# Kernel tuning notes

Measured on AMD Instinct MI355X. Metric: run time of the kernel, lower is better.

Reference implementation:

```python
import jax, jax.numpy as jnp
import numpy as np

EPS = 1e-5  # torch BatchNorm1d default eps

def lrelu(v):
    # LeakyReLU(0.2)
    return jnp.where(v >= 0, v, 0.2 * v)

def setup_inputs() -> dict:
    key = jax.random.key(0)
    ks = jax.random.split(key, 5)
    B, C, N = 32, 64, 1024  # batch, in_features(=out_features), num_nodes
    def w(k, shape, scale):
        return (jax.random.normal(k, shape) * scale).astype(jnp.float32)
    return {
        "x": jax.random.normal(ks[0], (B, C, N), jnp.float32),
        # static_adj: Conv1d(N, N, 1, bias=False) -> weight [N, N]
        "W_sa": w(ks[1], (N, N), 0.02),
        # static_weight: Conv1d(C, C, 1) -> weight [C, C], bias [C]
        "W_sw": w(ks[2], (C, C), 0.1),
        "b_sw": jnp.zeros((C,), jnp.float32),
        # bn: BatchNorm1d(64) affine params (training-mode batch stats used)
        "bn_gamma": jnp.ones((C,), jnp.float32),
        "bn_beta": jnp.zeros((C,), jnp.float32),
        # gamma parameter (init 0 in torch; set 0.5 so the attention path is live)
        "gamma": jnp.full((1,), 0.5, jnp.float32),
        # conv_create_co_mat: Conv1d(C, N, 1) -> weight [N, C], bias [N]
        "W_cm": w(ks[3], (N, C), 0.1),
        "b_cm": jnp.zeros((N,), jnp.float32),
        # dynamic_weight: Conv1d(C, C, 1) -> weight [C, C], bias [C]
        "W_dw": w(ks[4], (C, C), 0.1),
        "b_dw": jnp.zeros((C,), jnp.float32),
    }

def reference(x, W_sa, W_sw, b_sw, bn_gamma, bn_beta, gamma, W_cm, b_cm, W_dw, b_dw):
    # x: [B, C, N]
    # ---- static GCN: adj mix over nodes, then 1x1 conv over channels ----
    t = lrelu(jnp.einsum('mn,bcn->bcm', W_sa, x))                     # [B, C, N]
    out_static = lrelu(jnp.einsum('oc,bcn->bon', W_sw, t) + b_sw[None, :, None])
    x1 = x + out_static                                               # [B, C, N]
    # ---- construct dynamic graph ----
    energy = jnp.einsum('bcn,bdn->bcd', x, x)                         # [B, C, C]
    energy_new = jnp.max(energy, axis=-1, keepdims=True) - energy     # [B, C, C]
    # BatchNorm1d(64) in training mode: batch stats over (B, last) per channel
    mu = jnp.mean(energy_new, axis=(0, 2), keepdims=True)
    var = jnp.var(energy_new, axis=(0, 2), keepdims=True)
    attention = bn_gamma[None, :, None] * (energy_new - mu) * jax.lax.rsqrt(var + EPS) + bn_beta[None, :, None]
    out = jnp.einsum('bcd,bdn->bcn', attention, x)                    # [B, C, N]
    x_glb = gamma * out + x
    dyn_adj = jax.nn.sigmoid(jnp.einsum('mc,bcn->bmn', W_cm, x_glb) + b_cm[None, :, None])  # [B, N, N]
    # ---- dynamic GCN ----
    y = lrelu(jnp.einsum('bcn,bnm->bcm', x1, dyn_adj))                # [B, C, N]
    y = lrelu(jnp.einsum('oc,bcn->bon', W_dw, y) + b_dw[None, :, None])
    return y
```

## Files before the change

### kernel.cpp

```cpp
#include <hip/hip_runtime.h>
#include <hip/hip_bf16.h>

#define Bv 32
#define Cv 64
#define Nv 1024

typedef __attribute__((ext_vector_type(8))) short bf16x8;
typedef __attribute__((ext_vector_type(4))) float f32x4;
typedef __attribute__((ext_vector_type(8))) unsigned short us8;
typedef __attribute__((ext_vector_type(4))) unsigned short us4;

__device__ __forceinline__ float lrelu(float v) { return v >= 0.f ? v : 0.2f * v; }
__device__ __forceinline__ float sigmoidf_(float z) {
  return __builtin_amdgcn_rcpf(1.f + __expf(-z));
}
__device__ __forceinline__ unsigned short f2bh(float f) {
  __hip_bfloat16 h = __float2bfloat16(f);
  return reinterpret_cast<unsigned short&>(h);
}
__device__ __forceinline__ void gload16(const void* g, void* l) {
  __builtin_amdgcn_global_load_lds((const __attribute__((address_space(1))) void*)g,
                                   (__attribute__((address_space(3))) void*)l, 16, 0, 0);
}
__device__ __forceinline__ void stage_tile(const unsigned short* src, size_t stride,
                                           unsigned short* dst, int wave, int lane) {
#pragma unroll
  for (int p = 0; p < 2; ++p) {
    int q = wave * 2 + p;
    int rr = q * 8 + (lane >> 3);
    int gS = ((lane & 7) ^ (rr & 7)) << 3;
    gload16(&src[(size_t)rr * stride + gS], &dst[q * 512]);
  }
}
__device__ __forceinline__ bf16x8 fragr(const unsigned short* buf, int row, int ks, int lane) {
  return *reinterpret_cast<const bf16x8*>(
      &buf[row * 64 + (((ks * 4 + (lane >> 4)) ^ (row & 7)) << 3)]);
}

__device__ __forceinline__ void cvt8(const float* in, unsigned short* out, int i) {
  const f32x4* p = reinterpret_cast<const f32x4*>(in + (size_t)i * 8);
  f32x4 a = p[0], b = p[1];
  us8 o;
  o[0] = f2bh(a[0]); o[1] = f2bh(a[1]); o[2] = f2bh(a[2]); o[3] = f2bh(a[3]);
  o[4] = f2bh(b[0]); o[5] = f2bh(b[1]); o[6] = f2bh(b[2]); o[7] = f2bh(b[3]);
  *reinterpret_cast<us8*>(out + (size_t)i * 8) = o;
}

__global__ __launch_bounds__(256)
void prep_kernel(const float* __restrict__ x, const float* __restrict__ Wsa,
                 const float* __restrict__ Wcm, const float* __restrict__ Wsw,
                 const float* __restrict__ Wdw, unsigned short* __restrict__ xb,
                 unsigned short* __restrict__ xbT, unsigned short* __restrict__ WsaB,
                 unsigned short* __restrict__ WcmB, unsigned short* __restrict__ WswB,
                 unsigned short* __restrict__ WdwB) {
  __shared__ unsigned short L[64 * 72];
  const int blk = blockIdx.x, tid = threadIdx.x;
  if (blk < 512) {
    int b = blk >> 4, n0 = (blk & 15) * 64;
    int c = tid >> 2, nseg = (tid & 3) * 16;
    const float* src = &x[((size_t)(b * 64 + c) << 10) + n0 + nseg];
    unsigned short v16[16];
#pragma unroll
    for (int q = 0; q < 4; ++q) {
      f32x4 v = *reinterpret_cast<const f32x4*>(src + q * 4);
#pragma unroll
      for (int e = 0; e < 4; ++e) {
        unsigned short bf = f2bh(v[e]);
        v16[q * 4 + e] = bf;
        L[(nseg + q * 4 + e) * 72 + c] = bf;
      }
    }
    unsigned short* sd = &xb[((size_t)(b * 64 + c) << 10) + n0 + nseg];
    *reinterpret_cast<us8*>(sd) = *reinterpret_cast<const us8*>(&v16[0]);
    *reinterpret_cast<us8*>(sd + 8) = *reinterpret_cast<const us8*>(&v16[8]);
    __syncthreads();
    int n = tid >> 2, cs = (tid & 3) * 16;
    us8 a = *reinterpret_cast<const us8*>(&L[n * 72 + cs]);
    us8 bq = *reinterpret_cast<const us8*>(&L[n * 72 + cs + 8]);
    unsigned short* dst = &xbT[(((size_t)b << 10) + n0 + n) * 64 + cs];
    *reinterpret_cast<us8*>(dst) = a;
    *reinterpret_cast<us8*>(dst + 8) = bq;
  } else if (blk < 1024) {
    cvt8(Wsa, WsaB, (blk - 512) * 256 + tid);
  } else if (blk < 1056) {
    cvt8(Wcm, WcmB, (blk - 1024) * 256 + tid);
  } else if (blk < 1058) {
    cvt8(Wsw, WswB, (blk - 1056) * 256 + tid);
  } else {
    cvt8(Wdw, WdwB, (blk - 1058) * 256 + tid);
  }
}

__global__ __launch_bounds__(256)
void k1x1_kernel(const unsigned short* __restrict__ xb,
                 const unsigned short* __restrict__ WsaB,
                 const unsigned short* __restrict__ WswB,
                 const float* __restrict__ x, const float* __restrict__ bsw,
                 unsigned short* __restrict__ x1b, float* __restrict__ en) {
  __shared__ __align__(16) unsigned short As[2][4096];
  __shared__ __align__(16) unsigned short Bs[2][4096];
  __shared__ __align__(16) unsigned short TT[64 * 72];
  __shared__ __align__(16) float Xres[64 * 68];
  const int tid = threadIdx.x, wave = tid >> 6, lane = tid & 63;
  const int b = blockIdx.y, col0 = blockIdx.x * 64, row0 = b * 64;
  const int wr = wave >> 1, wc = wave & 1;
  const bool doEn = (blockIdx.x == 0);
  f32x4 acc[2][2], accE[4];
#pragma unroll
  for (int i = 0; i < 2; ++i)
#pragma unroll
    for (int j = 0; j < 2; ++j) acc[i][j] = (f32x4){0.f, 0.f, 0.f, 0.f};
#pragma unroll
  for (int j = 0; j < 4; ++j) accE[j] = (f32x4){0.f, 0.f, 0.f, 0.f};

  stage_tile(&xb[(size_t)row0 * Nv], Nv, As[0], wave, lane);
  stage_tile(&WsaB[(size_t)col0 * Nv], Nv, Bs[0], wave, lane);
  __syncthreads();
  for (int t = 0; t < 16; ++t) {
    const int cur = t & 1;
    if (t < 15) {
      stage_tile(&xb[(size_t)row0 * Nv + (t + 1) * 64], Nv, As[cur ^ 1], wave, lane);
      stage_tile(&WsaB[(size_t)col0 * Nv + (t + 1) * 64], Nv, Bs[cur ^ 1], wave, lane);
    }
#pragma unroll
    for (int ks = 0; ks < 2; ++ks) {
      bf16x8 af[2], bfg[2];
#pragma unroll
      for (int i = 0; i < 2; ++i) af[i] = fragr(As[cur], wr * 32 + i * 16 + (lane & 15), ks, lane);
#pragma unroll
      for (int j = 0; j < 2; ++j) bfg[j] = fragr(Bs[cur], wc * 32 + j * 16 + (lane & 15), ks, lane);
#pragma unroll
      for (int i = 0; i < 2; ++i)
#pragma unroll
        for (int j = 0; j < 2; ++j)
          acc[i][j] = __builtin_amdgcn_mfma_f32_16x16x32_bf16(af[i], bfg[j], acc[i][j], 0, 0, 0);
      if (doEn) {
        bf16x8 aE = fragr(As[cur], wave * 16 + (lane & 15), ks, lane);
#pragma unroll
        for (int j = 0; j < 4; ++j) {
          bf16x8 bE = fragr(As[cur], j * 16 + (lane & 15), ks, lane);
          accE[j] = __builtin_amdgcn_mfma_f32_16x16x32_bf16(aE, bE, accE[j], 0, 0, 0);
        }
      }
    }
    __syncthreads();
  }
#pragma unroll
  for (int i = 0; i < 2; ++i)
#pragma unroll
    for (int j = 0; j < 2; ++j) {
      us4 tv;
#pragma unroll
      for (int r = 0; r < 4; ++r) tv[r] = f2bh(lrelu(acc[i][j][r]));
      *reinterpret_cast<us4*>(
          &TT[(wc * 32 + j * 16 + (lane & 15)) * 72 + wr * 32 + i * 16 + (lane >> 4) * 4]) = tv;
    }
  {
    int o = tid >> 2, ms = (tid & 3) * 16;
    const float* xs = &x[((size_t)(row0 + o) << 10) + col0 + ms];
#pragma unroll
    for (int q = 0; q < 4; ++q)
      *reinterpret_cast<f32x4*>(&Xres[o * 68 + ms + q * 4]) =
          *reinterpret_cast<const f32x4*>(xs + q * 4);
  }
  if (doEn) {
#pragma unroll
    for (int j = 0; j < 4; ++j)
#pragma unroll
      for (int r = 0; r < 4; ++r)
        en[(size_t)b * 4096 + (wave * 16 + (lane >> 4) * 4 + r) * 64 + j * 16 + (lane & 15)] =
            accE[j][r];
  }
  __syncthreads();
  bf16x8 afw[2];
#pragma unroll
  for (int ks = 0; ks < 2; ++ks)
    afw[ks] = *reinterpret_cast<const bf16x8*>(
        &WswB[(wave * 16 + (lane & 15)) * 64 + ks * 32 + (lane >> 4) * 8]);
  f32x4 acc2[4];
#pragma unroll
  for (int j = 0; j < 4; ++j) acc2[j] = (f32x4){0.f, 0.f, 0.f, 0.f};
#pragma unroll
  for (int ks = 0; ks < 2; ++ks)
#pragma unroll
    for (int j = 0; j < 4; ++j) {
      bf16x8 bfr = *reinterpret_cast<const bf16x8*>(
          &TT[(j * 16 + (lane & 15)) * 72 + ks * 32 + (lane >> 4) * 8]);
      acc2[j] = __builtin_amdgcn_mfma_f32_16x16x32_bf16(afw[ks], bfr, acc2[j], 0, 0, 0);
    }
  f32x4 bs4 = *reinterpret_cast<const f32x4*>(&bsw[wave * 16 + (lane >> 4) * 4]);
#pragma unroll
  for (int j = 0; j < 4; ++j)
#pragma unroll
    for (int r = 0; r < 4; ++r) {
      int o = wave * 16 + (lane >> 4) * 4 + r;
      int nl = j * 16 + (lane & 15);
      x1b[((size_t)(row0 + o) << 10) + col0 + nl] =
          f2bh(Xres[o * 68 + nl] + lrelu(acc2[j][r] + bs4[r]));
    }
}

__global__ __launch_bounds__(64)
void bn_att_kernel(const float* __restrict__ en, const float* __restrict__ bng,
                   const float* __restrict__ bnb, unsigned short* __restrict__ att) {
  const int c = blockIdx.x, d = threadIdx.x;
  float v[Bv];
  float sum = 0.f, sumsq = 0.f;
#pragma unroll
  for (int b = 0; b < Bv; ++b) {
    float e = en[(size_t)b * 4096 + c * 64 + d];
    float m = e;
#pragma unroll
    for (int o = 32; o > 0; o >>= 1) m = fmaxf(m, __shfl_xor(m, o));
    v[b] = m - e;
    sum += v[b]; sumsq += v[b] * v[b];
  }
#pragma unroll
  for (int o = 32; o > 0; o >>= 1) { sum += __shfl_xor(sum, o); sumsq += __shfl_xor(sumsq, o); }
  const float inv = 1.f / (float)(Bv * Cv);
  float mu = sum * inv;
  float var = sumsq * inv - mu * mu;
  float rs = rsqrtf(var + 1e-5f);
  float g = bng[c], be = bnb[c];
#pragma unroll
  for (int b = 0; b < Bv; ++b)
    att[(size_t)b * 4096 + c * 64 + d] = f2bh(g * (v[b] - mu) * rs + be);
}

__global__ __launch_bounds__(256)
void dynmega_kernel(const unsigned short* __restrict__ xbT,
                    const unsigned short* __restrict__ x1b,
                    const unsigned short* __restrict__ attB,
                    const unsigned short* __restrict__ WcmB,
                    const unsigned short* __restrict__ WdwB,
                    const float* __restrict__ x, const float* __restrict__ bcm,
                    const float* __restrict__ bdw, const float* __restrict__ gamma_p,
                    float* __restrict__ dout) {
  __shared__ __align__(16) unsigned short XG[64 * 72];
  __shared__ __align__(16) char buf[32768];
  __shared__ __align__(16) unsigned short SBt[4 * 16 * 72];
  const int tid = threadIdx.x, wave = tid >> 6, lane = tid & 63;
  const int m0 = blockIdx.x * 64, b = blockIdx.y;
  {
    unsigned short* XB = (unsigned short*)buf;
    float* Xr = (float*)(buf + 8192);
    stage_tile(&xbT[((size_t)b * 1024 + m0) * 64], 64, XB, wave, lane);
    {
      int o = tid >> 2, ms = (tid & 3) * 16;
      const float* xs = &x[((size_t)(b * 64 + o) << 10) + m0 + ms];
#pragma unroll
      for (int q = 0; q < 4; ++q)
        *reinterpret_cast<f32x4*>(&Xr[o * 68 + ms + q * 4]) =
            *reinterpret_cast<const f32x4*>(xs + q * 4);
    }
    __syncthreads();
    bf16x8 afA[2];
#pragma unroll
    for (int ks = 0; ks < 2; ++ks)
      afA[ks] = *reinterpret_cast<const bf16x8*>(
          &attB[(size_t)b * 4096 + (wave * 16 + (lane & 15)) * 64 + ks * 32 + (lane >> 4) * 8]);
    const float g0 = gamma_p[0];
#pragma unroll
    for (int j = 0; j < 4; ++j) {
      f32x4 ah = (f32x4){0.f, 0.f, 0.f, 0.f};
#pragma unroll
      for (int ks = 0; ks < 2; ++ks) {
        bf16x8 bfh = fragr(XB, j * 16 + (lane & 15), ks, lane);
        ah = __builtin_amdgcn_mfma_f32_16x16x32_bf16(afA[ks], bfh, ah, 0, 0, 0);
      }
      us4 gv;
#pragma unroll
      for (int r = 0; r < 4; ++r)
        gv[r] =
            f2bh(g0 * ah[r] + Xr[(wave * 16 + (lane >> 4) * 4 + r) * 68 + j * 16 + (lane & 15)]);
      *reinterpret_cast<us4*>(
          &XG[(j * 16 + (lane & 15)) * 72 + wave * 16 + (lane >> 4) * 4]) = gv;
    }
  }
  __syncthreads();
  bf16x8 xgf[2];
#pragma unroll
  for (int ks = 0; ks < 2; ++ks)
    xgf[ks] = *reinterpret_cast<const bf16x8*>(
        &XG[(wave * 16 + (lane & 15)) * 72 + ks * 32 + (lane >> 4) * 8]);
  stage_tile(&WcmB[0], 64, (unsigned short*)buf, wave, lane);
  stage_tile(&x1b[(size_t)b * 65536], 1024, (unsigned short*)(buf + 8192), wave, lane);
  __syncthreads();
  f32x4 accy[4];
#pragma unroll
  for (int j = 0; j < 4; ++j) accy[j] = (f32x4){0.f, 0.f, 0.f, 0.f};
  unsigned short* SB = &SBt[wave * 16 * 72];

  auto chunk_body = [&](const char* base, int ch) {
    const unsigned short* WTcur = (const unsigned short*)base;
    const unsigned short* X1cur = (const unsigned short*)(base + 8192);
#pragma unroll
    for (int i = 0; i < 4; ++i) {
      f32x4 s = (f32x4){0.f, 0.f, 0.f, 0.f};
#pragma unroll
      for (int ks = 0; ks < 2; ++ks) {
        bf16x8 af = fragr(WTcur, i * 16 + (lane & 15), ks, lane);
        s = __builtin_amdgcn_mfma_f32_16x16x32_bf16(af, xgf[ks], s, 0, 0, 0);
      }
      f32x4 bc4 = *reinterpret_cast<const f32x4*>(&bcm[ch * 64 + i * 16 + (lane >> 4) * 4]);
      us4 sv;
#pragma unroll
      for (int r = 0; r < 4; ++r) sv[r] = f2bh(sigmoidf_(s[r] + bc4[r]));
      *reinterpret_cast<us4*>(&SB[(lane & 15) * 72 + i * 16 + (lane >> 4) * 4]) = sv;
    }
#pragma unroll
    for (int ks = 0; ks < 2; ++ks) {
      bf16x8 b2 = *reinterpret_cast<const bf16x8*>(
          &SB[(lane & 15) * 72 + ks * 32 + (lane >> 4) * 8]);
#pragma unroll
      for (int jc = 0; jc < 4; ++jc) {
        bf16x8 a2 = fragr(X1cur, jc * 16 + (lane & 15), ks, lane);
        accy[jc] = __builtin_amdgcn_mfma_f32_16x16x32_bf16(a2, b2, accy[jc], 0, 0, 0);
      }
    }
  };

  for (int hp = 0; hp < 8; ++hp) {
    {
      const int ch = hp * 2;
      stage_tile(&WcmB[(size_t)(ch + 1) * 4096], 64, (unsigned short*)(buf + 16384), wave, lane);
      stage_tile(&x1b[(size_t)b * 65536 + (ch + 1) * 64], 1024,
                 (unsigned short*)(buf + 16384 + 8192), wave, lane);
      chunk_body(buf, ch);
      __syncthreads();
    }
    {
      const int ch = hp * 2 + 1;
      if (hp < 7) {
        stage_tile(&WcmB[(size_t)(ch + 1) * 4096], 64, (unsigned short*)buf, wave, lane);
        stage_tile(&x1b[(size_t)b * 65536 + (ch + 1) * 64], 1024,
                   (unsigned short*)(buf + 8192), wave, lane);
      }
      chunk_body(buf + 16384, ch);
      __syncthreads();
    }
  }
  unsigned short* YT = SB;
#pragma unroll
  for (int jc = 0; jc < 4; ++jc) {
    us4 yv;
#pragma unroll
    for (int r = 0; r < 4; ++r) yv[r] = f2bh(lrelu(accy[jc][r]));
    *reinterpret_cast<us4*>(&YT[(lane & 15) * 72 + jc * 16 + (lane >> 4) * 4]) = yv;
  }
  bf16x8 afW[4][2];
#pragma unroll
  for (int jo = 0; jo < 4; ++jo)
#pragma unroll
    for (int ks = 0; ks < 2; ++ks)
      afW[jo][ks] = *reinterpret_cast<const bf16x8*>(
          &WdwB[(jo * 16 + (lane & 15)) * 64 + ks * 32 + (lane >> 4) * 8]);
  f32x4 accf[4];
#pragma unroll
  for (int j = 0; j < 4; ++j) accf[j] = (f32x4){0.f, 0.f, 0.f, 0.f};
#pragma unroll
  for (int ks = 0; ks < 2; ++ks) {
    bf16x8 yf = *reinterpret_cast<const bf16x8*>(
        &YT[(lane & 15) * 72 + ks * 32 + (lane >> 4) * 8]);
#pragma unroll
    for (int jo = 0; jo < 4; ++jo)
      accf[jo] = __builtin_amdgcn_mfma_f32_16x16x32_bf16(afW[jo][ks], yf, accf[jo], 0, 0, 0);
  }
#pragma unroll
  for (int jo = 0; jo < 4; ++jo) {
    f32x4 bs4 = *reinterpret_cast<const f32x4*>(&bdw[jo * 16 + (lane >> 4) * 4]);
#pragma unroll
    for (int r = 0; r < 4; ++r) {
      int o = jo * 16 + (lane >> 4) * 4 + r;
      dout[((size_t)(b * 64 + o) << 10) + m0 + wave * 16 + (lane & 15)] =
          lrelu(accf[jo][r] + bs4[r]);
    }
  }
}

extern "C" void kernel_launch(void* const* d_in, const int* in_sizes, int n_in,
                              void* d_out, int out_size, void* d_ws, size_t ws_size,
                              hipStream_t stream) {
  const float* x     = (const float*)d_in[0];
  const float* W_sa  = (const float*)d_in[1];
  const float* W_sw  = (const float*)d_in[2];
  const float* b_sw  = (const float*)d_in[3];
  const float* bn_g  = (const float*)d_in[4];
  const float* bn_b  = (const float*)d_in[5];
  const float* gamma = (const float*)d_in[6];
  const float* W_cm  = (const float*)d_in[7];
  const float* b_cm  = (const float*)d_in[8];
  const float* W_dw  = (const float*)d_in[9];
  const float* b_dw  = (const float*)d_in[10];
  float* out = (float*)d_out;

  char* ws = (char*)d_ws;
  const size_t MB = 1024 * 1024;
  unsigned short* xb     = (unsigned short*)(ws + 0 * MB);
  unsigned short* xbT    = (unsigned short*)(ws + 4 * MB);
  unsigned short* WsaB   = (unsigned short*)(ws + 8 * MB);
  unsigned short* WcmB   = (unsigned short*)(ws + 10 * MB);
  unsigned short* WswB   = (unsigned short*)(ws + 10 * MB + 256 * 1024);
  unsigned short* WdwB   = (unsigned short*)(ws + 10 * MB + 288 * 1024);
  unsigned short* x1b    = (unsigned short*)(ws + 11 * MB);
  float*          en     = (float*)(ws + 15 * MB);
  unsigned short* attB   = (unsigned short*)(ws + 16 * MB);

  prep_kernel<<<1060, 256, 0, stream>>>(x, W_sa, W_cm, W_sw, W_dw, xb, xbT, WsaB, WcmB, WswB,
                                        WdwB);
  k1x1_kernel<<<dim3(16, Bv), 256, 0, stream>>>(xb, WsaB, WswB, x, b_sw, x1b, en);
  bn_att_kernel<<<Cv, 64, 0, stream>>>(en, bn_g, bn_b, attB);
  dynmega_kernel<<<dim3(16, Bv), 256, 0, stream>>>(xbT, x1b, attB, WcmB, WdwB, x, b_cm, b_dw,
                                                   gamma, out);
}
```

Baseline: 58.93 us.

## Widen dynamic GCN block to 128 nodes with 8 waves sharing staged tiles

The dynamic megakernel now runs 512 threads per block covering 128 output nodes instead of 64. The staged W_cm and x1 chunk tiles are shared by twice as many waves, which halves redundant global and LDS staging per output. LDS padding is replaced by XOR swizzle so the larger buffers fit, and the residual x is read directly from global memory instead of being staged in LDS. The grid halves to 256 blocks, which may lower occupancy across CUs, and the uncoalesced direct x loads could cost bandwidth.

```diff
diff --git a/kernel.cpp b/kernel.cpp
--- a/kernel.cpp
+++ b/kernel.cpp
@@ -32,9 +32,18 @@
     gload16(&src[(size_t)rr * stride + gS], &dst[q * 512]);
   }
 }
+__device__ __forceinline__ void stage_tile8(const unsigned short* src, size_t stride,
+                                            unsigned short* dst, int wave, int lane) {
+  int rr = wave * 8 + (lane >> 3);
+  int gS = ((lane & 7) ^ (rr & 7)) << 3;
+  gload16(&src[(size_t)rr * stride + gS], &dst[wave * 512]);
+}
 __device__ __forceinline__ bf16x8 fragr(const unsigned short* buf, int row, int ks, int lane) {
   return *reinterpret_cast<const bf16x8*>(
       &buf[row * 64 + (((ks * 4 + (lane >> 4)) ^ (row & 7)) << 3)]);
+}
+__device__ __forceinline__ void swz_store4(unsigned short* buf, int row, int col, us4 v) {
+  *reinterpret_cast<us4*>(&buf[row * 64 + (((col >> 3) ^ (row & 7)) << 3) + (col & 7)]) = v;
 }
 
 __device__ __forceinline__ void cvt8(const float* in, unsigned short* out, int i) {
@@ -227,7 +236,7 @@
     att[(size_t)b * 4096 + c * 64 + d] = f2bh(g * (v[b] - mu) * rs + be);
 }
 
-__global__ __launch_bounds__(256)
+__global__ __launch_bounds__(512)
 void dynmega_kernel(const unsigned short* __restrict__ xbT,
                     const unsigned short* __restrict__ x1b,
                     const unsigned short* __restrict__ attB,
@@ -236,60 +245,55 @@
                     const float* __restrict__ x, const float* __restrict__ bcm,
                     const float* __restrict__ bdw, const float* __restrict__ gamma_p,
                     float* __restrict__ dout) {
-  __shared__ __align__(16) unsigned short XG[64 * 72];
+  __shared__ __align__(16) unsigned short XG[128 * 64];
   __shared__ __align__(16) char buf[32768];
-  __shared__ __align__(16) unsigned short SBt[4 * 16 * 72];
+  __shared__ __align__(16) unsigned short SBt[8 * 16 * 64];
   const int tid = threadIdx.x, wave = tid >> 6, lane = tid & 63;
-  const int m0 = blockIdx.x * 64, b = blockIdx.y;
+  const int M0 = blockIdx.x * 128, b = blockIdx.y;
   {
     unsigned short* XB = (unsigned short*)buf;
-    float* Xr = (float*)(buf + 8192);
-    stage_tile(&xbT[((size_t)b * 1024 + m0) * 64], 64, XB, wave, lane);
-    {
-      int o = tid >> 2, ms = (tid & 3) * 16;
-      const float* xs = &x[((size_t)(b * 64 + o) << 10) + m0 + ms];
-#pragma unroll
-      for (int q = 0; q < 4; ++q)
-        *reinterpret_cast<f32x4*>(&Xr[o * 68 + ms + q * 4]) =
-            *reinterpret_cast<const f32x4*>(xs + q * 4);
-    }
+    stage_tile8(&xbT[((size_t)b * 1024 + M0) * 64], 64, XB, wave, lane);
+    stage_tile8(&xbT[((size_t)b * 1024 + M0 + 64) * 64], 64, XB + 4096, wave, lane);
     __syncthreads();
+    const int cs = (wave & 3) * 16, mt = wave >> 2;
+    const unsigned short* XBm = XB + mt * 4096;
     bf16x8 afA[2];
 #pragma unroll
     for (int ks = 0; ks < 2; ++ks)
       afA[ks] = *reinterpret_cast<const bf16x8*>(
-          &attB[(size_t)b * 4096 + (wave * 16 + (lane & 15)) * 64 + ks * 32 + (lane >> 4) * 8]);
+          &attB[(size_t)b * 4096 + (cs + (lane & 15)) * 64 + ks * 32 + (lane >> 4) * 8]);
     const float g0 = gamma_p[0];
 #pragma unroll
     for (int j = 0; j < 4; ++j) {
       f32x4 ah = (f32x4){0.f, 0.f, 0.f, 0.f};
 #pragma unroll
       for (int ks = 0; ks < 2; ++ks) {
-        bf16x8 bfh = fragr(XB, j * 16 + (lane & 15), ks, lane);
+        bf16x8 bfh = fragr(XBm, j * 16 + (lane & 15), ks, lane);
         ah = __builtin_amdgcn_mfma_f32_16x16x32_bf16(afA[ks], bfh, ah, 0, 0, 0);
       }
+      const int mrow = mt * 64 + j * 16 + (lane & 15);
       us4 gv;
 #pragma unroll
-      for (int r = 0; r < 4; ++r)
-        gv[r] =
-            f2bh(g0 * ah[r] + Xr[(wave * 16 + (lane >> 4) * 4 + r) * 68 + j * 16 + (lane & 15)]);
-      *reinterpret_cast<us4*>(
-          &XG[(j * 16 + (lane & 15)) * 72 + wave * 16 + (lane >> 4) * 4]) = gv;
+      for (int r = 0; r < 4; ++r) {
+        int c = cs + (lane >> 4) * 4 + r;
+        float xr = x[((size_t)(b * 64 + c) << 10) + M0 + mrow];
+        gv[r] = f2bh(g0 * ah[r] + xr);
+      }
+      swz_store4(XG, mrow, cs + (lane >> 4) * 4, gv);
     }
   }
   __syncthreads();
   bf16x8 xgf[2];
 #pragma unroll
   for (int ks = 0; ks < 2; ++ks)
-    xgf[ks] = *reinterpret_cast<const bf16x8*>(
-        &XG[(wave * 16 + (lane & 15)) * 72 + ks * 32 + (lane >> 4) * 8]);
-  stage_tile(&WcmB[0], 64, (unsigned short*)buf, wave, lane);
-  stage_tile(&x1b[(size_t)b * 65536], 1024, (unsigned short*)(buf + 8192), wave, lane);
+    xgf[ks] = fragr(XG, wave * 16 + (lane & 15), ks, lane);
+  stage_tile8(&WcmB[0], 64, (unsigned short*)buf, wave, lane);
+  stage_tile8(&x1b[(size_t)b * 65536], 1024, (unsigned short*)(buf + 8192), wave, lane);
   __syncthreads();
   f32x4 accy[4];
 #pragma unroll
   for (int j = 0; j < 4; ++j) accy[j] = (f32x4){0.f, 0.f, 0.f, 0.f};
-  unsigned short* SB = &SBt[wave * 16 * 72];
+  unsigned short* SB = &SBt[wave * 1024];
 
   auto chunk_body = [&](const char* base, int ch) {
     const unsigned short* WTcur = (const unsigned short*)base;
@@ -306,12 +310,11 @@
       us4 sv;
 #pragma unroll
       for (int r = 0; r < 4; ++r) sv[r] = f2bh(sigmoidf_(s[r] + bc4[r]));
-      *reinterpret_cast<us4*>(&SB[(lane & 15) * 72 + i * 16 + (lane >> 4) * 4]) = sv;
+      swz_store4(SB, lane & 15, i * 16 + (lane >> 4) * 4, sv);
     }
 #pragma unroll
     for (int ks = 0; ks < 2; ++ks) {
-      bf16x8 b2 = *reinterpret_cast<const bf16x8*>(
-          &SB[(lane & 15) * 72 + ks * 32 + (lane >> 4) * 8]);
+      bf16x8 b2 = fragr(SB, lane & 15, ks, lane);
 #pragma unroll
       for (int jc = 0; jc < 4; ++jc) {
         bf16x8 a2 = fragr(X1cur, jc * 16 + (lane & 15), ks, lane);
@@ -323,30 +326,29 @@
   for (int hp = 0; hp < 8; ++hp) {
     {
       const int ch = hp * 2;
-      stage_tile(&WcmB[(size_t)(ch + 1) * 4096], 64, (unsigned short*)(buf + 16384), wave, lane);
-      stage_tile(&x1b[(size_t)b * 65536 + (ch + 1) * 64], 1024,
-                 (unsigned short*)(buf + 16384 + 8192), wave, lane);
+      stage_tile8(&WcmB[(size_t)(ch + 1) * 4096], 64, (unsigned short*)(buf + 16384), wave, lane);
+      stage_tile8(&x1b[(size_t)b * 65536 + (ch + 1) * 64], 1024,
+                  (unsigned short*)(buf + 16384 + 8192), wave, lane);
       chunk_body(buf, ch);
       __syncthreads();
     }
     {
       const int ch = hp * 2 + 1;
       if (hp < 7) {
-        stage_tile(&WcmB[(size_t)(ch + 1) * 4096], 64, (unsigned short*)buf, wave, lane);
-        stage_tile(&x1b[(size_t)b * 65536 + (ch + 1) * 64], 1024,
-                   (unsigned short*)(buf + 8192), wave, lane);
+        stage_tile8(&WcmB[(size_t)(ch + 1) * 4096], 64, (unsigned short*)buf, wave, lane);
+        stage_tile8(&x1b[(size_t)b * 65536 + (ch + 1) * 64], 1024,
+                    (unsigned short*)(buf + 8192), wave, lane);
       }
       chunk_body(buf + 16384, ch);
       __syncthreads();
     }
   }
-  unsigned short* YT = SB;
 #pragma unroll
   for (int jc = 0; jc < 4; ++jc) {
     us4 yv;
 #pragma unroll
     for (int r = 0; r < 4; ++r) yv[r] = f2bh(lrelu(accy[jc][r]));
-    *reinterpret_cast<us4*>(&YT[(lane & 15) * 72 + jc * 16 + (lane >> 4) * 4]) = yv;
+    swz_store4(SB, lane & 15, jc * 16 + (lane >> 4) * 4, yv);
   }
   bf16x8 afW[4][2];
 #pragma unroll
@@ -360,8 +362,7 @@
   for (int j = 0; j < 4; ++j) accf[j] = (f32x4){0.f, 0.f, 0.f, 0.f};
 #pragma unroll
   for (int ks = 0; ks < 2; ++ks) {
-    bf16x8 yf = *reinterpret_cast<const bf16x8*>(
-        &YT[(lane & 15) * 72 + ks * 32 + (lane >> 4) * 8]);
+    bf16x8 yf = fragr(SB, lane & 15, ks, lane);
 #pragma unroll
     for (int jo = 0; jo < 4; ++jo)
       accf[jo] = __builtin_amdgcn_mfma_f32_16x16x32_bf16(afW[jo][ks], yf, accf[jo], 0, 0, 0);
@@ -372,7 +373,7 @@
 #pragma unroll
     for (int r = 0; r < 4; ++r) {
       int o = jo * 16 + (lane >> 4) * 4 + r;
-      dout[((size_t)(b * 64 + o) << 10) + m0 + wave * 16 + (lane & 15)] =
+      dout[((size_t)(b * 64 + o) << 10) + M0 + wave * 16 + (lane & 15)] =
           lrelu(accf[jo][r] + bs4[r]);
     }
   }
@@ -410,6 +411,6 @@
                                         WdwB);
   k1x1_kernel<<<dim3(16, Bv), 256, 0, stream>>>(xb, WsaB, WswB, x, b_sw, x1b, en);
   bn_att_kernel<<<Cv, 64, 0, stream>>>(en, bn_g, bn_b, attB);
-  dynmega_kernel<<<dim3(16, Bv), 256, 0, stream>>>(xbT, x1b, attB, WcmB, WdwB, x, b_cm, b_dw,
-                                                   gamma, out);
-}
+  dynmega_kernel<<<dim3(8, Bv), 512, 0, stream>>>(xbT, x1b, attB, WcmB, WdwB, x, b_cm, b_dw,
+                                                  gamma, out);
+}
```

Result: slower. 60.61 us (+2.9%).

## Triple-buffer dynamic GCN chunk staging with vmcnt waits and single barrier

Applied to the files above, without the earlier changes.

Replaces the double-buffered chunk loop in the dynamic kernel with a three-slot ring buffer. Loads are issued two chunks ahead and waited on with explicit s_waitcnt vmcnt counts followed by a raw s_barrier, so each chunk needs one barrier instead of a full __syncthreads. The intent is to hide more global-to-LDS latency behind the MFMA work. The cost is 16KB more LDS per block, which may lower occupancy. Correctness relies on the vmcnt count matching the four loads issued per stage_chunk.

```diff
diff --git a/kernel.cpp b/kernel.cpp
--- a/kernel.cpp
+++ b/kernel.cpp
@@ -22,6 +22,9 @@
   __builtin_amdgcn_global_load_lds((const __attribute__((address_space(1))) void*)g,
                                    (__attribute__((address_space(3))) void*)l, 16, 0, 0);
 }
+__device__ __forceinline__ void wait_vm4() { asm volatile("s_waitcnt vmcnt(4)" ::: "memory"); }
+__device__ __forceinline__ void wait_vm0() { asm volatile("s_waitcnt vmcnt(0)" ::: "memory"); }
+
 __device__ __forceinline__ void stage_tile(const unsigned short* src, size_t stride,
                                            unsigned short* dst, int wave, int lane) {
 #pragma unroll
@@ -237,7 +240,7 @@
                     const float* __restrict__ bdw, const float* __restrict__ gamma_p,
                     float* __restrict__ dout) {
   __shared__ __align__(16) unsigned short XG[64 * 72];
-  __shared__ __align__(16) char buf[32768];
+  __shared__ __align__(16) char buf[49152];
   __shared__ __align__(16) unsigned short SBt[4 * 16 * 72];
   const int tid = threadIdx.x, wave = tid >> 6, lane = tid & 63;
   const int m0 = blockIdx.x * 64, b = blockIdx.y;
@@ -283,14 +286,16 @@
   for (int ks = 0; ks < 2; ++ks)
     xgf[ks] = *reinterpret_cast<const bf16x8*>(
         &XG[(wave * 16 + (lane & 15)) * 72 + ks * 32 + (lane >> 4) * 8]);
-  stage_tile(&WcmB[0], 64, (unsigned short*)buf, wave, lane);
-  stage_tile(&x1b[(size_t)b * 65536], 1024, (unsigned short*)(buf + 8192), wave, lane);
-  __syncthreads();
   f32x4 accy[4];
 #pragma unroll
   for (int j = 0; j < 4; ++j) accy[j] = (f32x4){0.f, 0.f, 0.f, 0.f};
   unsigned short* SB = &SBt[wave * 16 * 72];
 
+  auto stage_chunk = [&](int ch, char* slot) {
+    stage_tile(&WcmB[(size_t)ch * 4096], 64, (unsigned short*)slot, wave, lane);
+    stage_tile(&x1b[(size_t)b * 65536 + ch * 64], 1024, (unsigned short*)(slot + 8192), wave,
+               lane);
+  };
   auto chunk_body = [&](const char* base, int ch) {
     const unsigned short* WTcur = (const unsigned short*)base;
     const unsigned short* X1cur = (const unsigned short*)(base + 8192);
@@ -319,27 +324,23 @@
       }
     }
   };
-
-  for (int hp = 0; hp < 8; ++hp) {
-    {
-      const int ch = hp * 2;
-      stage_tile(&WcmB[(size_t)(ch + 1) * 4096], 64, (unsigned short*)(buf + 16384), wave, lane);
-      stage_tile(&x1b[(size_t)b * 65536 + (ch + 1) * 64], 1024,
-                 (unsigned short*)(buf + 16384 + 8192), wave, lane);
-      chunk_body(buf, ch);
-      __syncthreads();
-    }
-    {
-      const int ch = hp * 2 + 1;
-      if (hp < 7) {
-        stage_tile(&WcmB[(size_t)(ch + 1) * 4096], 64, (unsigned short*)buf, wave, lane);
-        stage_tile(&x1b[(size_t)b * 65536 + (ch + 1) * 64], 1024,
-                   (unsigned short*)(buf + 8192), wave, lane);
-      }
-      chunk_body(buf + 16384, ch);
-      __syncthreads();
-    }
-  }
+  auto pipe_iter = [&](int ch, int curslot, int nxtslot) {
+    if (ch < 15) wait_vm4(); else wait_vm0();
+    __builtin_amdgcn_s_barrier();
+    if (ch + 2 <= 15) stage_chunk(ch + 2, buf + nxtslot * 16384);
+    chunk_body(buf + curslot * 16384, ch);
+  };
+
+  stage_chunk(0, buf);
+  stage_chunk(1, buf + 16384);
+#pragma unroll
+  for (int g = 0; g < 5; ++g) {
+    pipe_iter(3 * g + 0, 0, 2);
+    pipe_iter(3 * g + 1, 1, 0);
+    pipe_iter(3 * g + 2, 2, 1);
+  }
+  pipe_iter(15, 0, 2);
+
   unsigned short* YT = SB;
 #pragma unroll
   for (int jc = 0; jc < 4; ++jc) {
```

Result: slower. 60.38 us (+2.5%).
